# Kernel optimization log

Hardware: AMD Instinct MI355X
Metric: run time of the kernel (lower is better)

## Reference

```python
import jax, jax.numpy as jnp
import numpy as np

N_NODES = 20000
K = 8                      # forward offsets per node; total degree = 2K = 16
IN_FEAT = 128
HID = 256
OUT_FEAT = 1
EPS = 1e-5


def _build_graph():
    # Regular undirected graph: node i -> (i+o) % N for o in 1..K, plus reverse edges.
    base = np.repeat(np.arange(N_NODES), K)
    off = np.tile(np.arange(1, K + 1), N_NODES)
    d = (base + off) % N_NODES
    src = np.concatenate([base, d]).astype(np.int32)   # [E], E = 2*N*K
    dst = np.concatenate([d, base]).astype(np.int32)
    deg = 2 * K
    # Every node has exactly `deg` out-edges and `deg` in-edges -> reshape works.
    out_ids = np.argsort(src, kind='stable').reshape(N_NODES, deg)  # edges leaving v
    in_ids = np.argsort(dst, kind='stable').reshape(N_NODES, deg)   # edges entering v
    # Directed line graph: edge (a,v) -> edge (v,c): pair every in-edge with every out-edge of v.
    line_src = np.repeat(in_ids, deg, axis=1).ravel().astype(np.int32)
    line_dst = np.tile(out_ids, (1, deg)).ravel().astype(np.int32)
    return np.stack([src, dst]), np.stack([line_src, line_dst])


def setup_inputs() -> dict:
    key = jax.random.key(0)
    ks = jax.random.split(key, 4)
    ei, lei = _build_graph()
    x = jax.random.normal(ks[0], (N_NODES, IN_FEAT), jnp.float32)
    W1 = jax.random.normal(ks[1], (IN_FEAT, HID), jnp.float32) / np.sqrt(IN_FEAT).astype(np.float32)
    b1 = jnp.zeros((HID,), jnp.float32)
    gamma1 = jnp.ones((HID,), jnp.float32)
    beta1 = jnp.zeros((HID,), jnp.float32)
    W2 = jax.random.normal(ks[2], (HID, HID), jnp.float32) / np.sqrt(HID).astype(np.float32)
    b2 = jnp.zeros((HID,), jnp.float32)
    Wl = jax.random.normal(ks[3], (2 * HID, OUT_FEAT), jnp.float32) / np.sqrt(2 * HID).astype(np.float32)
    bl = jnp.zeros((OUT_FEAT,), jnp.float32)
    return {"x": x, "W1": W1, "b1": b1, "gamma1": gamma1, "beta1": beta1,
            "W2": W2, "b2": b2, "Wl": Wl, "bl": bl,
            "edge_index": jnp.asarray(ei), "line_edge_index": jnp.asarray(lei)}


def _gcn(x, edge_index, W, b, n):
    # GCNConv: add self loops, symmetric deg^{-1/2} normalization, sum aggregation.
    h = x @ W                                                  # [n, out]
    loops = jnp.arange(n, dtype=edge_index.dtype)
    src = jnp.concatenate([edge_index[0], loops])
    dst = jnp.concatenate([edge_index[1], loops])
    deg = jax.ops.segment_sum(jnp.ones(src.shape, h.dtype), dst, num_segments=n)
    dinv = jnp.where(deg > 0, jax.lax.rsqrt(jnp.maximum(deg, 1.0)), 0.0)
    norm = dinv[src] * dinv[dst]                               # [E+n]
    return jax.ops.segment_sum(h[src] * norm[:, None], dst, num_segments=n) + b


def _batch_norm(x, gamma, beta):
    mu = x.mean(axis=0)
    var = x.var(axis=0)
    return (x - mu) * jax.lax.rsqrt(var + EPS) * gamma + beta


def reference(x, W1, b1, gamma1, beta1, W2, b2, Wl, bl, edge_index, line_edge_index):
    n = x.shape[0]
    h = jax.nn.relu(_batch_norm(_gcn(x, edge_index, W1, b1, n), gamma1, beta1))
    h = jax.nn.relu(_gcn(h, edge_index, W2, b2, n))
    # to_line_graph, node_feat_mixing='cat': one line-node per edge, feat = [x_src | x_dst]
    line_x = jnp.concatenate([h[edge_index[0]], h[edge_index[1]]], axis=1)  # [E, 2*HID]
    out = _gcn(line_x, line_edge_index, Wl, bl, line_x.shape[0])
    return jax.nn.sigmoid(out)
```

## Files before the change

### kernel.cpp

```cpp
#include <hip/hip_runtime.h>
#include <hip/hip_bf16.h>
#include <math.h>

#define NN    20000
#define NK    160000
#define NEDGE 320000
#define HID   256
#define INFEAT 128
#define EPSF  1e-5f
#define NT1B  157
#define MOUT  104
#define NT2B  193

typedef __bf16  bf16x8 __attribute__((ext_vector_type(8)));
typedef float   f32x4  __attribute__((ext_vector_type(4)));
typedef ushort  u16x8  __attribute__((ext_vector_type(8)));

__device__ __forceinline__ float sigmoidf_(float x) { return 1.0f / (1.0f + expf(-x)); }

__device__ __forceinline__ ushort f2bf(float f) {
    __hip_bfloat16 h = __float2bfloat16(f);
    return __builtin_bit_cast(ushort, h);
}
__device__ __forceinline__ float bf2f(ushort u) {
    return __builtin_bit_cast(float, ((unsigned int)u) << 16);
}
__device__ __forceinline__ int wrapN(int v) {
    return (v < 0) ? v + NN : ((v >= NN) ? v - NN : v);
}

#define LDSP(p) ((__attribute__((address_space(3))) unsigned int*)(p))
#define GBLP(p) ((const __attribute__((address_space(1))) unsigned int*)(p))
#define GLD16(g, l) __builtin_amdgcn_global_load_lds(GBLP(g), LDSP(l), 16, 0, 0)

__device__ __forceinline__ u16x8 bnrelu8(const u16x8 a, const float* ssS, int fb) {
    const float4 sc0 = *reinterpret_cast<const float4*>(ssS + fb);
    const float4 sc1 = *reinterpret_cast<const float4*>(ssS + fb + 4);
    const float4 sh0 = *reinterpret_cast<const float4*>(ssS + 256 + fb);
    const float4 sh1 = *reinterpret_cast<const float4*>(ssS + 256 + fb + 4);
    u16x8 p;
    p[0] = f2bf(fmaxf(bf2f(a[0]) * sc0.x + sh0.x, 0.f));
    p[1] = f2bf(fmaxf(bf2f(a[1]) * sc0.y + sh0.y, 0.f));
    p[2] = f2bf(fmaxf(bf2f(a[2]) * sc0.z + sh0.z, 0.f));
    p[3] = f2bf(fmaxf(bf2f(a[3]) * sc0.w + sh0.w, 0.f));
    p[4] = f2bf(fmaxf(bf2f(a[4]) * sc1.x + sh1.x, 0.f));
    p[5] = f2bf(fmaxf(bf2f(a[5]) * sc1.y + sh1.y, 0.f));
    p[6] = f2bf(fmaxf(bf2f(a[6]) * sc1.z + sh1.z, 0.f));
    p[7] = f2bf(fmaxf(bf2f(a[7]) * sc1.w + sh1.w, 0.f));
    return p;
}

__device__ __forceinline__ u16x8 pack8(const float4 a, const float4 b) {
    u16x8 p;
    p[0] = f2bf(a.x); p[1] = f2bf(a.y); p[2] = f2bf(a.z); p[3] = f2bf(a.w);
    p[4] = f2bf(b.x); p[5] = f2bf(b.y); p[6] = f2bf(b.z); p[7] = f2bf(b.w);
    return p;
}

__global__ __launch_bounds__(512, 2) void k_prep(const float* __restrict__ W1,
    const float* __restrict__ W2, ushort* __restrict__ W1t,
    ushort* __restrict__ W2t, float* __restrict__ asum)
{
    const int b = blockIdx.x, t = threadIdx.x;
    if (b < 16) {
        const int e = (b * 512 + t) * 4;
        ushort4 o;
        #pragma unroll
        for (int j = 0; j < 4; ++j) {
            const int ee = e + j;
            const int n = ee >> 7, k = ee & 127;
            ((ushort*)&o)[j] = f2bf(W1[k * 256 + n]);
        }
        *reinterpret_cast<ushort4*>(W1t + e) = o;
    } else if (b < 48) {
        const int e = ((b - 16) * 512 + t) * 4;
        ushort4 o;
        #pragma unroll
        for (int j = 0; j < 4; ++j) {
            const int ee = e + j;
            const int n = ee >> 8, k = ee & 255;
            ((ushort*)&o)[j] = f2bf(W2[k * 256 + n]);
        }
        *reinterpret_cast<ushort4*>(W2t + e) = o;
    } else {
        asum[t]       = 0.f;
        asum[512 + t] = 0.f;
    }
}

__global__ __launch_bounds__(1024, 4) void k_fused1(const float* __restrict__ x,
    const ushort* __restrict__ W1t, const float* __restrict__ b1,
    ushort* __restrict__ A, float* __restrict__ asum)
{
    __shared__ alignas(16) char smem[23040 + 16384 + 32768];
    char* xr = smem;
    char* As = smem + 23040;
    char* Bs = smem + 23040 + 16384;

    const int t = threadIdx.x;
    const int wave = t >> 6, lane = t & 63;
    const int wr  = (wave >> 2) * 32;
    const int wc4 = (wave & 3) * 64;
    const int bm = blockIdx.x * 128;
    const float inv17 = 1.0f / 17.0f;
    f32x4 acc[2][4] = {};

    const int rw0 = wrapN(bm - 8 + (t >> 3)),          c80 = (t & 7) * 8;
    const int rw1 = wrapN(bm - 8 + ((1024 + t) >> 3)), c81 = ((1024 + t) & 7) * 8;
    const bool v1 = t < 128;

    float4 xa0 = *reinterpret_cast<const float4*>(x + (size_t)rw0 * INFEAT + c80);
    float4 xa1 = *reinterpret_cast<const float4*>(x + (size_t)rw0 * INFEAT + c80 + 4);
    float4 xb0 = v1 ? *reinterpret_cast<const float4*>(x + (size_t)rw1 * INFEAT + c81)
                    : make_float4(0.f, 0.f, 0.f, 0.f);
    float4 xb1 = v1 ? *reinterpret_cast<const float4*>(x + (size_t)rw1 * INFEAT + c81 + 4)
                    : make_float4(0.f, 0.f, 0.f, 0.f);

    #pragma unroll
    for (int kt = 0; kt < 2; ++kt) {
        const int k0 = kt * 64;
        *reinterpret_cast<u16x8*>(xr + (t >> 3) * 160 + (t & 7) * 16) = pack8(xa0, xa1);
        if (v1)
            *reinterpret_cast<u16x8*>(xr + ((1024 + t) >> 3) * 160 + ((1024 + t) & 7) * 16) = pack8(xb0, xb1);
        __syncthreads();
        #pragma unroll
        for (int it = 0; it < 2; ++it) {
            const int cb = (it * 16 + wave) * 64 + lane;
            const int row = cb >> 3;
            const int lk = (cb & 7) ^ (row & 7);
            GLD16(W1t + (size_t)row * INFEAT + k0 + lk * 8, Bs + (it * 16 + wave) * 1024);
        }
        {
            const int row = t >> 3, c8 = t & 7;
            float S[8] = {};
            #pragma unroll
            for (int i = 0; i < 17; ++i) {
                const u16x8 h = *reinterpret_cast<const u16x8*>(xr + (row + i) * 160 + c8 * 16);
                #pragma unroll
                for (int j = 0; j < 8; ++j) S[j] += bf2f(h[j]);
            }
            u16x8 o;
            #pragma unroll
            for (int j = 0; j < 8; ++j) o[j] = f2bf(S[j] * inv17);
            *reinterpret_cast<u16x8*>(As + row * 128 + ((c8 ^ (row & 7)) * 16)) = o;
        }
        __syncthreads();
        if (kt == 0) {
            xa0 = *reinterpret_cast<const float4*>(x + (size_t)rw0 * INFEAT + 64 + c80);
            xa1 = *reinterpret_cast<const float4*>(x + (size_t)rw0 * INFEAT + 64 + c80 + 4);
            if (v1) {
                xb0 = *reinterpret_cast<const float4*>(x + (size_t)rw1 * INFEAT + 64 + c81);
                xb1 = *reinterpret_cast<const float4*>(x + (size_t)rw1 * INFEAT + 64 + c81 + 4);
            }
        }
        __builtin_amdgcn_s_setprio(1);
        #pragma unroll
        for (int kk = 0; kk < 2; ++kk) {
            const int klog = kk * 64 + ((lane >> 4) << 4);
            bf16x8 af[2];
            #pragma unroll
            for (int mi = 0; mi < 2; ++mi) {
                const int row = wr + mi * 16 + (lane & 15);
                af[mi] = *reinterpret_cast<const bf16x8*>(As + row * 128 + (klog ^ ((row & 7) << 4)));
            }
            #pragma unroll
            for (int ni = 0; ni < 4; ++ni) {
                const int rl = wc4 + ni * 16 + (lane & 15);
                const bf16x8 bv = *reinterpret_cast<const bf16x8*>(Bs + rl * 128 + (klog ^ ((rl & 7) << 4)));
                #pragma unroll
                for (int mi = 0; mi < 2; ++mi)
                    acc[mi][ni] = __builtin_amdgcn_mfma_f32_16x16x32_bf16(af[mi], bv, acc[mi][ni], 0, 0, 0);
            }
        }
        __builtin_amdgcn_s_setprio(0);
    }

    float* sS  = (float*)smem;
    float* s2S = (float*)(smem + 4096);
    #pragma unroll
    for (int ni = 0; ni < 4; ++ni) {
        const int colL = wc4 + ni * 16 + (lane & 15);
        const float bv = b1[colL];
        float sv = 0.f, s2v = 0.f;
        #pragma unroll
        for (int mi = 0; mi < 2; ++mi)
            #pragma unroll
            for (int r = 0; r < 4; ++r) {
                const int row = bm + wr + mi * 16 + ((lane >> 4) << 2) + r;
                if (row < NN) {
                    const float val = acc[mi][ni][r] + bv;
                    A[(size_t)row * 256 + colL] = f2bf(val);
                    sv += val; s2v += val * val;
                }
            }
        sv  += __shfl_xor(sv, 16);  sv  += __shfl_xor(sv, 32);
        s2v += __shfl_xor(s2v, 16); s2v += __shfl_xor(s2v, 32);
        if (lane < 16) {
            sS [wave * 64 + ni * 16 + lane] = sv;
            s2S[wave * 64 + ni * 16 + lane] = s2v;
        }
    }
    __syncthreads();
    if (t < 256) {
        const int col = t;
        const int g = col >> 6, idx = col & 63;
        float s = 0.f, s2 = 0.f;
        #pragma unroll
        for (int wv = g; wv < 16; wv += 4) {
            s  += sS [wv * 64 + idx];
            s2 += s2S[wv * 64 + idx];
        }
        atomicAdd(&asum[col],       s);
        atomicAdd(&asum[512 + col], s2);
    }
}

__global__ __launch_bounds__(1024, 4) void k_fused2(const ushort* __restrict__ A,
    const ushort* __restrict__ W2t, const float* __restrict__ gamma,
    const float* __restrict__ beta, const float* __restrict__ b2,
    const float* __restrict__ Wl, const float* __restrict__ bl,
    const float* __restrict__ asum, float* __restrict__ out)
{
    __shared__ alignas(16) char smem[23040 + 16384 + 32768 + 2048];
    char* xr   = smem;
    char* As   = smem + 23040;
    char* Bs   = smem + 23040 + 16384;
    float* ssS = (float*)(smem + 23040 + 16384 + 32768);

    const int b = blockIdx.x, t = threadIdx.x;
    const int wave = t >> 6, lane = t & 63;
    const int wr  = (wave >> 2) * 32;
    const int wc4 = (wave & 3) * 64;
    const int v0 = b * MOUT;
    const float inv17 = 1.0f / 17.0f;

    if (t < 256) {
        const float invn = 1.0f / (float)NN;
        const float mu  = asum[t] * invn;
        const float var = asum[512 + t] * invn - mu * mu;
        const float sc  = gamma[t] * rsqrtf(var + EPSF);
        ssS[t]       = sc;
        ssS[256 + t] = beta[t] - mu * sc;
    }
    __syncthreads();

    f32x4 acc[2][4] = {};

    const int rg0 = wrapN(v0 - 16 + (t >> 3)),          f80 = (t & 7) * 8;
    const int rg1 = wrapN(v0 - 16 + ((1024 + t) >> 3)), f81 = ((1024 + t) & 7) * 8;
    const bool v1 = t < 128;

    u16x8 aq0 = *reinterpret_cast<const u16x8*>(A + (size_t)rg0 * 256 + f80);
    u16x8 aq1 = v1 ? *reinterpret_cast<const u16x8*>(A + (size_t)rg1 * 256 + f81)
                   : u16x8{};

    #pragma unroll
    for (int kt = 0; kt < 4; ++kt) {
        const int k0 = kt * 64;
        *reinterpret_cast<u16x8*>(xr + (t >> 3) * 160 + (t & 7) * 16)
            = bnrelu8(aq0, ssS, k0 + f80);
        if (v1)
            *reinterpret_cast<u16x8*>(xr + ((1024 + t) >> 3) * 160 + ((1024 + t) & 7) * 16)
                = bnrelu8(aq1, ssS, k0 + f81);
        __syncthreads();
        #pragma unroll
        for (int it = 0; it < 2; ++it) {
            const int cb = (it * 16 + wave) * 64 + lane;
            const int row = cb >> 3;
            const int lk = (cb & 7) ^ (row & 7);
            GLD16(W2t + (size_t)row * 256 + k0 + lk * 8, Bs + (it * 16 + wave) * 1024);
        }
        {
            const int row = t >> 3, c8 = t & 7;
            float S[8] = {};
            #pragma unroll
            for (int i = 0; i < 17; ++i) {
                const u16x8 h = *reinterpret_cast<const u16x8*>(xr + (row + i) * 160 + c8 * 16);
                #pragma unroll
                for (int j = 0; j < 8; ++j) S[j] += bf2f(h[j]);
            }
            u16x8 o;
            #pragma unroll
            for (int j = 0; j < 8; ++j) o[j] = f2bf(S[j] * inv17);
            *reinterpret_cast<u16x8*>(As + row * 128 + ((c8 ^ (row & 7)) * 16)) = o;
        }
        __syncthreads();
        if (kt < 3) {
            const int k1 = k0 + 64;
            aq0 = *reinterpret_cast<const u16x8*>(A + (size_t)rg0 * 256 + k1 + f80);
            if (v1)
                aq1 = *reinterpret_cast<const u16x8*>(A + (size_t)rg1 * 256 + k1 + f81);
        }
        __builtin_amdgcn_s_setprio(1);
        #pragma unroll
        for (int kk = 0; kk < 2; ++kk) {
            const int klog = kk * 64 + ((lane >> 4) << 4);
            bf16x8 af[2];
            #pragma unroll
            for (int mi = 0; mi < 2; ++mi) {
                const int row = wr + mi * 16 + (lane & 15);
                af[mi] = *reinterpret_cast<const bf16x8*>(As + row * 128 + (klog ^ ((row & 7) << 4)));
            }
            #pragma unroll
            for (int ni = 0; ni < 4; ++ni) {
                const int rl = wc4 + ni * 16 + (lane & 15);
                const bf16x8 bv = *reinterpret_cast<const bf16x8*>(Bs + rl * 128 + (klog ^ ((rl & 7) << 4)));
                #pragma unroll
                for (int mi = 0; mi < 2; ++mi)
                    acc[mi][ni] = __builtin_amdgcn_mfma_f32_16x16x32_bf16(af[mi], bv, acc[mi][ni], 0, 0, 0);
            }
        }
        __builtin_amdgcn_s_setprio(0);
    }

    float b2v[4], wav[4], wbv[4];
    #pragma unroll
    for (int ni = 0; ni < 4; ++ni) {
        const int col = wc4 + ni * 16 + (lane & 15);
        b2v[ni] = b2[col];
        wav[ni] = Wl[col];
        wbv[ni] = Wl[256 + col];
    }
    float* uW = (float*)smem;
    float* wW = (float*)(smem + 2048);
    float* uL = (float*)(smem + 23040);
    float* wL = (float*)(smem + 23040 + 512);
    float* PS = (float*)(smem + 23040 + 1024);
    #pragma unroll
    for (int mi = 0; mi < 2; ++mi)
        #pragma unroll
        for (int r = 0; r < 4; ++r) {
            float pu = 0.f, pw = 0.f;
            #pragma unroll
            for (int ni = 0; ni < 4; ++ni) {
                const float hv = fmaxf(acc[mi][ni][r] + b2v[ni], 0.f);
                pu += hv * wav[ni];
                pw += hv * wbv[ni];
            }
            pu += __shfl_xor(pu, 1); pu += __shfl_xor(pu, 2);
            pu += __shfl_xor(pu, 4); pu += __shfl_xor(pu, 8);
            pw += __shfl_xor(pw, 1); pw += __shfl_xor(pw, 2);
            pw += __shfl_xor(pw, 4); pw += __shfl_xor(pw, 8);
            if ((lane & 15) == 0) {
                const int rl = wr + mi * 16 + ((lane >> 4) << 2) + r;
                uW[(wave & 3) * 128 + rl] = pu;
                wW[(wave & 3) * 128 + rl] = pw;
            }
        }
    __syncthreads();
    if (t < 128) {
        uL[t] = uW[t] + uW[128 + t] + uW[256 + t] + uW[384 + t];
        wL[t] = wW[t] + wW[128 + t] + wW[256 + t] + wW[384 + t];
    }
    __syncthreads();

    if (t < 112) {
        const int l = t + 8;
        float s = uL[l] + 16.0f * wL[l];
        #pragma unroll
        for (int o = 1; o <= 8; ++o)
            s += uL[l + o] + uL[l - o];
        PS[t] = s;
    }
    __syncthreads();

    const float blv = bl[0];
    #pragma unroll
    for (int rr = 0; rr < 2; ++rr) {
        const int q = t + rr * 1024;
        if (q >= 1664) continue;
        const int half = (q >= 832) ? 1 : 0;
        const int e = q - half * 832;
        const int i = e >> 3, off = e & 7;
        const int v = v0 + i;
        if (v >= NN) continue;
        if (!half) {
            out[v * 8 + off] = sigmoidf_((PS[i] + wL[i + 9 + off]) * inv17 + blv);
        } else {
            out[NK + v * 8 + off] = sigmoidf_((PS[i + 1 + off] + wL[i + 8]) * inv17 + blv);
        }
    }
}

extern "C" void kernel_launch(void* const* d_in, const int* in_sizes, int n_in,
                              void* d_out, int out_size, void* d_ws, size_t ws_size,
                              hipStream_t stream)
{
    const float* x      = (const float*)d_in[0];
    const float* W1     = (const float*)d_in[1];
    const float* b1     = (const float*)d_in[2];
    const float* gamma1 = (const float*)d_in[3];
    const float* beta1  = (const float*)d_in[4];
    const float* W2     = (const float*)d_in[5];
    const float* b2     = (const float*)d_in[6];
    const float* Wl     = (const float*)d_in[7];
    const float* bl     = (const float*)d_in[8];
    float* out = (float*)d_out;

    float*    asum = (float*)d_ws;
    ushort*   A    = (ushort*)(asum + 1024);
    ushort*   W1t  = A + (size_t)NN * 256;
    ushort*   W2t  = W1t + 256 * 128;

    k_prep  <<<49,   512,  0, stream>>>(W1, W2, W1t, W2t, asum);
    k_fused1<<<NT1B, 1024, 0, stream>>>(x, W1t, b1, A, asum);
    k_fused2<<<NT2B, 1024, 0, stream>>>(A, W2t, gamma1, beta1, b2, Wl, bl, asum, out);
}
```

Before: 43.70 us.

## Compute 17-row window sums via fp32 four-row partial sums in LDS

Replaces the direct 17-row neighbor-window sum with a two-stage scheme. Stage one builds four-row partial sums in a new fp32 LDS buffer. Stage two adds four partials plus one extra row per output. Staging input rows as fp32 instead of bf16 removes the pack/unpack conversions and cuts per-thread LDS reads. The cost is roughly 78 KB more shared memory per block, which likely limits occupancy to one block per CU, plus an extra barrier per k-tile.

Measured after the change: 42.59 us. 2.5% less time.

```diff
diff --git a/kernel.cpp b/kernel.cpp
--- a/kernel.cpp
+++ b/kernel.cpp
@@ -12,6 +12,8 @@
 #define MOUT  104
 #define NT2B  193
 
+#define XRS   272
+
 typedef __bf16  bf16x8 __attribute__((ext_vector_type(8)));
 typedef float   f32x4  __attribute__((ext_vector_type(4)));
 typedef ushort  u16x8  __attribute__((ext_vector_type(8)));
@@ -33,28 +35,47 @@
 #define GBLP(p) ((const __attribute__((address_space(1))) unsigned int*)(p))
 #define GLD16(g, l) __builtin_amdgcn_global_load_lds(GBLP(g), LDSP(l), 16, 0, 0)
 
-__device__ __forceinline__ u16x8 bnrelu8(const u16x8 a, const float* ssS, int fb) {
-    const float4 sc0 = *reinterpret_cast<const float4*>(ssS + fb);
-    const float4 sc1 = *reinterpret_cast<const float4*>(ssS + fb + 4);
-    const float4 sh0 = *reinterpret_cast<const float4*>(ssS + 256 + fb);
-    const float4 sh1 = *reinterpret_cast<const float4*>(ssS + 256 + fb + 4);
-    u16x8 p;
-    p[0] = f2bf(fmaxf(bf2f(a[0]) * sc0.x + sh0.x, 0.f));
-    p[1] = f2bf(fmaxf(bf2f(a[1]) * sc0.y + sh0.y, 0.f));
-    p[2] = f2bf(fmaxf(bf2f(a[2]) * sc0.z + sh0.z, 0.f));
-    p[3] = f2bf(fmaxf(bf2f(a[3]) * sc0.w + sh0.w, 0.f));
-    p[4] = f2bf(fmaxf(bf2f(a[4]) * sc1.x + sh1.x, 0.f));
-    p[5] = f2bf(fmaxf(bf2f(a[5]) * sc1.y + sh1.y, 0.f));
-    p[6] = f2bf(fmaxf(bf2f(a[6]) * sc1.z + sh1.z, 0.f));
-    p[7] = f2bf(fmaxf(bf2f(a[7]) * sc1.w + sh1.w, 0.f));
-    return p;
-}
-
-__device__ __forceinline__ u16x8 pack8(const float4 a, const float4 b) {
-    u16x8 p;
-    p[0] = f2bf(a.x); p[1] = f2bf(a.y); p[2] = f2bf(a.z); p[3] = f2bf(a.w);
-    p[4] = f2bf(b.x); p[5] = f2bf(b.y); p[6] = f2bf(b.z); p[7] = f2bf(b.w);
-    return p;
+__device__ __forceinline__ void bnrelu_f32(const u16x8 a, const float* ssS, int fb,
+                                           f32x4& o0, f32x4& o1) {
+    const f32x4 sc0 = *reinterpret_cast<const f32x4*>(ssS + fb);
+    const f32x4 sc1 = *reinterpret_cast<const f32x4*>(ssS + fb + 4);
+    const f32x4 sh0 = *reinterpret_cast<const f32x4*>(ssS + 256 + fb);
+    const f32x4 sh1 = *reinterpret_cast<const f32x4*>(ssS + 256 + fb + 4);
+    #pragma unroll
+    for (int j = 0; j < 4; ++j) {
+        o0[j] = fmaxf(bf2f(a[j])     * sc0[j] + sh0[j], 0.f);
+        o1[j] = fmaxf(bf2f(a[4 + j]) * sc1[j] + sh1[j], 0.f);
+    }
+}
+
+__device__ __forceinline__ void t4_item(const char* xr, char* t4, int r4, int c8) {
+    f32x4 s0 = {}, s1 = {};
+    #pragma unroll
+    for (int j = 0; j < 4; ++j) {
+        s0 += *reinterpret_cast<const f32x4*>(xr + (r4 + j) * XRS + c8 * 32);
+        s1 += *reinterpret_cast<const f32x4*>(xr + (r4 + j) * XRS + c8 * 32 + 16);
+    }
+    *reinterpret_cast<f32x4*>(t4 + r4 * XRS + c8 * 32)      = s0;
+    *reinterpret_cast<f32x4*>(t4 + r4 * XRS + c8 * 32 + 16) = s1;
+}
+
+__device__ __forceinline__ void as_item(const char* xr, const char* t4, char* As,
+                                        int row, int c8, float inv17) {
+    f32x4 s0 = *reinterpret_cast<const f32x4*>(t4 + row * XRS + c8 * 32);
+    f32x4 s1 = *reinterpret_cast<const f32x4*>(t4 + row * XRS + c8 * 32 + 16);
+    #pragma unroll
+    for (int m = 4; m <= 12; m += 4) {
+        s0 += *reinterpret_cast<const f32x4*>(t4 + (row + m) * XRS + c8 * 32);
+        s1 += *reinterpret_cast<const f32x4*>(t4 + (row + m) * XRS + c8 * 32 + 16);
+    }
+    s0 += *reinterpret_cast<const f32x4*>(xr + (row + 16) * XRS + c8 * 32);
+    s1 += *reinterpret_cast<const f32x4*>(xr + (row + 16) * XRS + c8 * 32 + 16);
+    u16x8 o;
+    #pragma unroll
+    for (int j = 0; j < 4; ++j) o[j]     = f2bf(s0[j] * inv17);
+    #pragma unroll
+    for (int j = 0; j < 4; ++j) o[4 + j] = f2bf(s1[j] * inv17);
+    *reinterpret_cast<u16x8*>(As + row * 128 + ((c8 ^ (row & 7)) * 16)) = o;
 }
 
 __global__ __launch_bounds__(512, 2) void k_prep(const float* __restrict__ W1,
@@ -92,10 +113,11 @@
     const ushort* __restrict__ W1t, const float* __restrict__ b1,
     ushort* __restrict__ A, float* __restrict__ asum)
 {
-    __shared__ alignas(16) char smem[23040 + 16384 + 32768];
+    __shared__ alignas(16) char smem[39168 + 39168 + 16384 + 32768];
     char* xr = smem;
-    char* As = smem + 23040;
-    char* Bs = smem + 23040 + 16384;
+    char* t4 = smem + 39168;
+    char* As = smem + 39168 + 39168;
+    char* Bs = smem + 39168 + 39168 + 16384;
 
     const int t = threadIdx.x;
     const int wave = t >> 6, lane = t & 63;
@@ -119,9 +141,16 @@
     #pragma unroll
     for (int kt = 0; kt < 2; ++kt) {
         const int k0 = kt * 64;
-        *reinterpret_cast<u16x8*>(xr + (t >> 3) * 160 + (t & 7) * 16) = pack8(xa0, xa1);
-        if (v1)
-            *reinterpret_cast<u16x8*>(xr + ((1024 + t) >> 3) * 160 + ((1024 + t) & 7) * 16) = pack8(xb0, xb1);
+        {
+            const int r0 = t >> 3, c8 = t & 7;
+            *reinterpret_cast<float4*>(xr + r0 * XRS + c8 * 32)      = xa0;
+            *reinterpret_cast<float4*>(xr + r0 * XRS + c8 * 32 + 16) = xa1;
+            if (v1) {
+                const int r1 = (1024 + t) >> 3, c81l = (1024 + t) & 7;
+                *reinterpret_cast<float4*>(xr + r1 * XRS + c81l * 32)      = xb0;
+                *reinterpret_cast<float4*>(xr + r1 * XRS + c81l * 32 + 16) = xb1;
+            }
+        }
         __syncthreads();
         #pragma unroll
         for (int it = 0; it < 2; ++it) {
@@ -130,20 +159,10 @@
             const int lk = (cb & 7) ^ (row & 7);
             GLD16(W1t + (size_t)row * INFEAT + k0 + lk * 8, Bs + (it * 16 + wave) * 1024);
         }
-        {
-            const int row = t >> 3, c8 = t & 7;
-            float S[8] = {};
-            #pragma unroll
-            for (int i = 0; i < 17; ++i) {
-                const u16x8 h = *reinterpret_cast<const u16x8*>(xr + (row + i) * 160 + c8 * 16);
-                #pragma unroll
-                for (int j = 0; j < 8; ++j) S[j] += bf2f(h[j]);
-            }
-            u16x8 o;
-            #pragma unroll
-            for (int j = 0; j < 8; ++j) o[j] = f2bf(S[j] * inv17);
-            *reinterpret_cast<u16x8*>(As + row * 128 + ((c8 ^ (row & 7)) * 16)) = o;
-        }
+        t4_item(xr, t4, t >> 3, t & 7);
+        if (v1) t4_item(xr, t4, 128 + (t >> 3), t & 7);
+        __syncthreads();
+        as_item(xr, t4, As, t >> 3, t & 7, inv17);
         __syncthreads();
         if (kt == 0) {
             xa0 = *reinterpret_cast<const float4*>(x + (size_t)rw0 * INFEAT + 64 + c80);
@@ -221,11 +240,12 @@
     const float* __restrict__ Wl, const float* __restrict__ bl,
     const float* __restrict__ asum, float* __restrict__ out)
 {
-    __shared__ alignas(16) char smem[23040 + 16384 + 32768 + 2048];
+    __shared__ alignas(16) char smem[39168 + 39168 + 16384 + 32768 + 2048];
     char* xr   = smem;
-    char* As   = smem + 23040;
-    char* Bs   = smem + 23040 + 16384;
-    float* ssS = (float*)(smem + 23040 + 16384 + 32768);
+    char* t4   = smem + 39168;
+    char* As   = smem + 39168 + 39168;
+    char* Bs   = smem + 39168 + 39168 + 16384;
+    float* ssS = (float*)(smem + 39168 + 39168 + 16384 + 32768);
 
     const int b = blockIdx.x, t = threadIdx.x;
     const int wave = t >> 6, lane = t & 63;
@@ -257,11 +277,19 @@
     #pragma unroll
     for (int kt = 0; kt < 4; ++kt) {
         const int k0 = kt * 64;
-        *reinterpret_cast<u16x8*>(xr + (t >> 3) * 160 + (t & 7) * 16)
-            = bnrelu8(aq0, ssS, k0 + f80);
-        if (v1)
-            *reinterpret_cast<u16x8*>(xr + ((1024 + t) >> 3) * 160 + ((1024 + t) & 7) * 16)
-                = bnrelu8(aq1, ssS, k0 + f81);
+        {
+            f32x4 o0, o1;
+            bnrelu_f32(aq0, ssS, k0 + f80, o0, o1);
+            const int r0 = t >> 3, c8 = t & 7;
+            *reinterpret_cast<f32x4*>(xr + r0 * XRS + c8 * 32)      = o0;
+            *reinterpret_cast<f32x4*>(xr + r0 * XRS + c8 * 32 + 16) = o1;
+            if (v1) {
+                bnrelu_f32(aq1, ssS, k0 + f81, o0, o1);
+                const int r1 = (1024 + t) >> 3, c81l = (1024 + t) & 7;
+                *reinterpret_cast<f32x4*>(xr + r1 * XRS + c81l * 32)      = o0;
+                *reinterpret_cast<f32x4*>(xr + r1 * XRS + c81l * 32 + 16) = o1;
+            }
+        }
         __syncthreads();
         #pragma unroll
         for (int it = 0; it < 2; ++it) {
@@ -270,20 +298,10 @@
             const int lk = (cb & 7) ^ (row & 7);
             GLD16(W2t + (size_t)row * 256 + k0 + lk * 8, Bs + (it * 16 + wave) * 1024);
         }
-        {
-            const int row = t >> 3, c8 = t & 7;
-            float S[8] = {};
-            #pragma unroll
-            for (int i = 0; i < 17; ++i) {
-                const u16x8 h = *reinterpret_cast<const u16x8*>(xr + (row + i) * 160 + c8 * 16);
-                #pragma unroll
-                for (int j = 0; j < 8; ++j) S[j] += bf2f(h[j]);
-            }
-            u16x8 o;
-            #pragma unroll
-            for (int j = 0; j < 8; ++j) o[j] = f2bf(S[j] * inv17);
-            *reinterpret_cast<u16x8*>(As + row * 128 + ((c8 ^ (row & 7)) * 16)) = o;
-        }
+        t4_item(xr, t4, t >> 3, t & 7);
+        if (v1) t4_item(xr, t4, 128 + (t >> 3), t & 7);
+        __syncthreads();
+        as_item(xr, t4, As, t >> 3, t & 7, inv17);
         __syncthreads();
         if (kt < 3) {
             const int k1 = k0 + 64;
```
